# Kernel optimization log

Hardware: AMD Instinct MI355X
Metric: run time of the kernel (lower is better)

Reference implementation:

```python
import jax, jax.numpy as jnp
import numpy as np

S = 256
H = 4       # n_heads
DH = 32     # head_dim
D = H * DH  # model dim
EPS = 1e-5


def setup_inputs() -> dict:
    key = jax.random.key(0)
    ks = jax.random.split(key, 12)
    x = jax.random.normal(ks[0], (1, S, S, D), dtype=jnp.float32)
    # attention mask: mostly 0, occasionally large negative (masked)
    keep = jax.random.uniform(ks[1], (1, 1, S, S)) < 0.9
    attn_mask = jnp.where(keep, 0.0, -1e9).astype(jnp.float32)
    sc = 1.0 / np.sqrt(D)
    ln_w = jnp.ones((D,), jnp.float32)
    ln_b = jnp.zeros((D,), jnp.float32)
    Wb = jax.random.normal(ks[2], (H, D), jnp.float32) * sc   # bias projection (linear.weight)
    Wq = jax.random.normal(ks[3], (D, D), jnp.float32) * sc
    Wk = jax.random.normal(ks[4], (D, D), jnp.float32) * sc
    Wv = jax.random.normal(ks[5], (D, D), jnp.float32) * sc
    Wg = jax.random.normal(ks[6], (D, D), jnp.float32) * sc
    Wo = jax.random.normal(ks[7], (D, D), jnp.float32) * sc
    return {"x": x, "attn_mask": attn_mask, "ln_w": ln_w, "ln_b": ln_b,
            "Wb": Wb, "Wq": Wq, "Wk": Wk, "Wv": Wv, "Wg": Wg, "Wo": Wo}


def reference(x, attn_mask, ln_w, ln_b, Wb, Wq, Wk, Wv, Wg, Wo):
    # x: [1,S,S,D] pair representation; ending=False so no transpose of S axes.
    x0 = x[0]  # [S,S,D]
    mu = jnp.mean(x0, axis=-1, keepdims=True)
    var = jnp.mean(jnp.square(x0 - mu), axis=-1, keepdims=True)
    xn = (x0 - mu) * jax.lax.rsqrt(var + EPS) * ln_w + ln_b  # [S,S,D]

    # triangle bias: [S,S,H] -> [1,H,S,S] (broadcast over batch-of-rows)
    bias = jnp.einsum('bqd,hd->hbq', xn, Wb)[None]  # [1,H,S,S]

    def heads(W):
        return jnp.einsum('bqd,ed->bqe', xn, W).reshape(S, S, H, DH).transpose(0, 2, 1, 3)

    q, k, v = heads(Wq), heads(Wk), heads(Wv)  # each [S,H,S,DH]

    scale = 1.0 / np.sqrt(DH)
    scores = jnp.einsum('bhqd,bhkd->bhqk', q, k) * scale + bias + attn_mask  # [S,H,S,S]
    attn = jax.nn.softmax(scores, axis=-1)
    o = jnp.einsum('bhqk,bhkd->bhqd', attn, v)  # [S,H,S,DH]
    o = o.transpose(0, 2, 1, 3).reshape(S, S, D)

    g = jnp.einsum('bqd,ed->bqe', xn, Wg)
    out = jnp.einsum('bqe,fe->bqf', o * jax.nn.sigmoid(g), Wo)  # [S,S,D]
    return out[None]  # [1,S,S,D]
```

## Files before the change

kernel.cpp:

```cpp
#include <hip/hip_runtime.h>
#include <hip/hip_bf16.h>

#define S_DIM 256
#define D_DIM 128
#define H_DIM 4
#define NPOS  (S_DIM * S_DIM)
#define SW    384

typedef __attribute__((ext_vector_type(8))) short  short8;
typedef __attribute__((ext_vector_type(4))) float  f32x4;

__device__ __forceinline__ float b2f(unsigned short u) {
    union { float f; unsigned int u32; } c; c.u32 = ((unsigned int)u) << 16; return c.f;
}
__device__ __forceinline__ unsigned short f2b(float f) {
    __hip_bfloat16 h = __float2bfloat16(f);
    return *reinterpret_cast<unsigned short*>(&h);
}

__global__ __launch_bounds__(256) void ln_biasmask_kernel(
    const float* __restrict__ x, const float* __restrict__ mask,
    const float* __restrict__ lnw, const float* __restrict__ lnb,
    const float* __restrict__ Wb, float* __restrict__ bm)
{
    const int wave = threadIdx.x >> 6, lane = threadIdx.x & 63;
    const int p = blockIdx.x * 4 + wave;

    float2 v = ((const float2*)x)[p * 64 + lane];
    float s = v.x + v.y, ss = v.x * v.x + v.y * v.y;
    #pragma unroll
    for (int m = 1; m < 64; m <<= 1) { s += __shfl_xor(s, m); ss += __shfl_xor(ss, m); }
    float mean = s * (1.f / 128.f);
    float var  = ss * (1.f / 128.f) - mean * mean;
    float rstd = rsqrtf(var + 1e-5f);

    float xn0 = (v.x - mean) * rstd * lnw[lane * 2]     + lnb[lane * 2];
    float xn1 = (v.y - mean) * rstd * lnw[lane * 2 + 1] + lnb[lane * 2 + 1];

    float mval = mask[p];
    #pragma unroll
    for (int h = 0; h < H_DIM; h++) {
        float d = xn0 * Wb[h * 128 + lane * 2] + xn1 * Wb[h * 128 + lane * 2 + 1];
        #pragma unroll
        for (int m = 1; m < 64; m <<= 1) d += __shfl_xor(d, m);
        if (lane == 0) bm[(long)h * NPOS + p] = d + mval;
    }
}

__global__ __launch_bounds__(256) void proj_ln_kernel(
    const float* __restrict__ x,
    const float* __restrict__ lnw, const float* __restrict__ lnb,
    const float* __restrict__ Wq, const float* __restrict__ Wk,
    const float* __restrict__ Wv, const float* __restrict__ Wg,
    int p0, unsigned short* __restrict__ strip, unsigned short* __restrict__ vt)
{
    __shared__ __align__(16) unsigned short A_lds[64 * 136];
    __shared__ __align__(16) unsigned short W_lds[128 * 136];
    const int tid = threadIdx.x;
    const int m0 = blockIdx.x * 64;
    const int gy = blockIdx.y;
    const float* W = (gy == 0) ? Wq : (gy == 1) ? Wk : (gy == 2) ? Wv : Wg;

    const int lr = tid >> 4, c8 = (tid & 15) * 8;
    #pragma unroll
    for (int i = 0; i < 4; i++) {
        int row = lr + i * 16;
        const float* src = x + (size_t)(p0 + m0 + row) * 128 + c8;
        float4 f0 = *(const float4*)(src);
        float4 f1 = *(const float4*)(src + 4);
        float s  = f0.x + f0.y + f0.z + f0.w + f1.x + f1.y + f1.z + f1.w;
        float ss = f0.x*f0.x + f0.y*f0.y + f0.z*f0.z + f0.w*f0.w
                 + f1.x*f1.x + f1.y*f1.y + f1.z*f1.z + f1.w*f1.w;
        #pragma unroll
        for (int m = 1; m < 16; m <<= 1) { s += __shfl_xor(s, m); ss += __shfl_xor(ss, m); }
        float mean = s * (1.f / 128.f);
        float var  = ss * (1.f / 128.f) - mean * mean;
        float rstd = rsqrtf(var + 1e-5f);
        float xv[8] = {f0.x, f0.y, f0.z, f0.w, f1.x, f1.y, f1.z, f1.w};
        unsigned short pk[8];
        #pragma unroll
        for (int j = 0; j < 8; j++)
            pk[j] = f2b((xv[j] - mean) * rstd * lnw[c8 + j] + lnb[c8 + j]);
        *(uint4*)(&A_lds[row * 136 + c8]) = *(const uint4*)pk;
    }
    #pragma unroll
    for (int i = 0; i < 8; i++) {
        int wr = lr + i * 16;
        const float* src = W + (size_t)wr * 128 + c8;
        float4 f0 = *(const float4*)(src);
        float4 f1 = *(const float4*)(src + 4);
        unsigned short pk[8] = {f2b(f0.x), f2b(f0.y), f2b(f0.z), f2b(f0.w),
                                f2b(f1.x), f2b(f1.y), f2b(f1.z), f2b(f1.w)};
        *(uint4*)(&W_lds[wr * 136 + c8]) = *(const uint4*)pk;
    }
    __syncthreads();

    const int w = tid >> 6, lane = tid & 63;
    const int l16 = lane & 15, quad = lane >> 4;
    f32x4 acc[8];
    #pragma unroll
    for (int nt = 0; nt < 8; nt++) acc[nt] = (f32x4){0.f, 0.f, 0.f, 0.f};

    if (gy == 2) {
        #pragma unroll
        for (int k0 = 0; k0 < 128; k0 += 32) {
            short8 a = *(const short8*)(&A_lds[(w * 16 + l16) * 136 + k0 + quad * 8]);
            #pragma unroll
            for (int nt = 0; nt < 8; nt++) {
                short8 b = *(const short8*)(&W_lds[(nt * 16 + l16) * 136 + k0 + quad * 8]);
                acc[nt] = __builtin_amdgcn_mfma_f32_16x16x32_bf16(a, b, acc[nt], 0, 0, 0);
            }
        }
        const int blv = m0 >> 8;
        const int kl  = (m0 & 255) + w * 16 + quad * 4;
        #pragma unroll
        for (int nt = 0; nt < 8; nt++) {
            uint2 pk;
            pk.x = (unsigned)f2b(acc[nt][0]) | ((unsigned)f2b(acc[nt][1]) << 16);
            pk.y = (unsigned)f2b(acc[nt][2]) | ((unsigned)f2b(acc[nt][3]) << 16);
            *(uint2*)(&vt[((size_t)(blv * 128 + nt * 16 + l16)) * 256 + kl]) = pk;
        }
    } else {
        #pragma unroll
        for (int k0 = 0; k0 < 128; k0 += 32) {
            short8 a = *(const short8*)(&A_lds[(w * 16 + l16) * 136 + k0 + quad * 8]);
            #pragma unroll
            for (int nt = 0; nt < 8; nt++) {
                short8 b = *(const short8*)(&W_lds[(nt * 16 + l16) * 136 + k0 + quad * 8]);
                acc[nt] = __builtin_amdgcn_mfma_f32_16x16x32_bf16(b, a, acc[nt], 0, 0, 0);
            }
        }
        const int off = (gy == 0) ? 0 : (gy == 1) ? 128 : 256;
        const size_t rowbase = (size_t)(m0 + w * 16 + l16) * SW + off;
        #pragma unroll
        for (int nt = 0; nt < 8; nt++) {
            uint2 pk;
            pk.x = (unsigned)f2b(acc[nt][0]) | ((unsigned)f2b(acc[nt][1]) << 16);
            pk.y = (unsigned)f2b(acc[nt][2]) | ((unsigned)f2b(acc[nt][3]) << 16);
            *(uint2*)(&strip[rowbase + nt * 16 + quad * 4]) = pk;
        }
    }
}

__global__ __launch_bounds__(256) void attn_kernel(
    const unsigned short* __restrict__ strip, const unsigned short* __restrict__ vt,
    const float* __restrict__ bm, int b0, unsigned short* __restrict__ gated)
{
    __shared__ __align__(16) unsigned short P_lds[4 * 16 * 264];
    const int bl = blockIdx.x, h = blockIdx.y;
    const int b  = b0 + bl;
    const int tid = threadIdx.x;
    const int w = tid >> 6, lane = tid & 63;
    const int l16 = lane & 15, quad = lane >> 4;
    const float* bmh = bm + (long)h * NPOS;
    const unsigned short* vth = vt + ((size_t)bl * 128 + h * 32) * 256;
    unsigned short* P_w = P_lds + w * 16 * 264;
    const float scale = 0.17677669529663687f;

    #pragma unroll 1
    for (int i = 0; i < 4; i++) {
        const int q0 = (w * 4 + i) * 16;
        short8 bq = *(const short8*)(strip + (size_t)(bl * 256 + q0 + l16) * SW + h * 32 + quad * 8);
        const float* brow = bmh + (size_t)(q0 + l16) * 256 + quad * 4;

        float sc[16][4];
        #pragma unroll
        for (int nt = 0; nt < 16; nt++) {
            short8 ka = *(const short8*)(strip + (size_t)(bl * 256 + nt * 16 + l16) * SW + 128 + h * 32 + quad * 8);
            f32x4 c = (f32x4){0.f, 0.f, 0.f, 0.f};
            c = __builtin_amdgcn_mfma_f32_16x16x32_bf16(ka, bq, c, 0, 0, 0);
            float4 bb = *(const float4*)(brow + nt * 16);
            sc[nt][0] = c[0] * scale + bb.x;
            sc[nt][1] = c[1] * scale + bb.y;
            sc[nt][2] = c[2] * scale + bb.z;
            sc[nt][3] = c[3] * scale + bb.w;
        }

        float m0 = sc[0][0], m1 = sc[0][1], m2 = sc[0][2], m3 = sc[0][3];
        #pragma unroll
        for (int nt = 1; nt < 16; nt++) {
            m0 = fmaxf(m0, sc[nt][0]); m1 = fmaxf(m1, sc[nt][1]);
            m2 = fmaxf(m2, sc[nt][2]); m3 = fmaxf(m3, sc[nt][3]);
        }
        float m = fmaxf(fmaxf(m0, m1), fmaxf(m2, m3));
        m = fmaxf(m, __shfl_xor(m, 16));
        m = fmaxf(m, __shfl_xor(m, 32));

        float s0 = 0.f, s1 = 0.f, s2 = 0.f, s3 = 0.f;
        #pragma unroll
        for (int nt = 0; nt < 16; nt++) {
            float p0_ = __expf(sc[nt][0] - m); sc[nt][0] = p0_; s0 += p0_;
            float p1_ = __expf(sc[nt][1] - m); sc[nt][1] = p1_; s1 += p1_;
            float p2_ = __expf(sc[nt][2] - m); sc[nt][2] = p2_; s2 += p2_;
            float p3_ = __expf(sc[nt][3] - m); sc[nt][3] = p3_; s3 += p3_;
        }
        float ssum = (s0 + s1) + (s2 + s3);
        ssum += __shfl_xor(ssum, 16);
        ssum += __shfl_xor(ssum, 32);
        float inv = 1.f / ssum;

        #pragma unroll
        for (int nt = 0; nt < 16; nt++) {
            uint2 pk;
            pk.x = (unsigned)f2b(sc[nt][0]) | ((unsigned)f2b(sc[nt][1]) << 16);
            pk.y = (unsigned)f2b(sc[nt][2]) | ((unsigned)f2b(sc[nt][3]) << 16);
            *(uint2*)(&P_w[l16 * 264 + nt * 16 + quad * 4]) = pk;
        }

        f32x4 oacc[2];
        oacc[0] = (f32x4){0.f, 0.f, 0.f, 0.f};
        oacc[1] = (f32x4){0.f, 0.f, 0.f, 0.f};
        #pragma unroll
        for (int kt = 0; kt < 8; kt++) {
            short8 pa = *(const short8*)(&P_w[l16 * 264 + kt * 32 + quad * 8]);
            #pragma unroll
            for (int nh = 0; nh < 2; nh++) {
                short8 vb = *(const short8*)(vth + (size_t)(nh * 16 + l16) * 256 + kt * 32 + quad * 8);
                oacc[nh] = __builtin_amdgcn_mfma_f32_16x16x32_bf16(pa, vb, oacc[nh], 0, 0, 0);
            }
        }
        #pragma unroll
        for (int rr = 0; rr < 4; rr++) {
            float invr = __shfl(inv, quad * 4 + rr);
            int row = q0 + quad * 4 + rr;
            #pragma unroll
            for (int nh = 0; nh < 2; nh++) {
                int cl = nh * 16 + l16;
                float g = b2f(strip[(size_t)(bl * 256 + row) * SW + 256 + h * 32 + cl]);
                float ov = oacc[nh][rr] * invr;
                ov = ov / (1.f + __expf(-g));
                gated[((size_t)b * 256 + row) * 128 + h * 32 + cl] = f2b(ov);
            }
        }
    }
}

__global__ __launch_bounds__(256) void outproj_mfma_kernel(
    const unsigned short* __restrict__ gated, const float* __restrict__ Wo,
    float* __restrict__ out)
{
    __shared__ __align__(16) unsigned short A_lds[64 * 136];
    __shared__ __align__(16) unsigned short W_lds[128 * 136];
    const int tid = threadIdx.x;
    const int m0 = blockIdx.x * 64;

    const int lr = tid >> 4, c8 = (tid & 15) * 8;
    #pragma unroll
    for (int i = 0; i < 4; i++) {
        int row = lr + i * 16;
        *(uint4*)(&A_lds[row * 136 + c8]) =
            *(const uint4*)(gated + (size_t)(m0 + row) * 128 + c8);
    }
    #pragma unroll
    for (int i = 0; i < 8; i++) {
        const float* src = Wo + (size_t)(lr + i * 16) * 128 + c8;
        float4 f0 = *(const float4*)(src);
        float4 f1 = *(const float4*)(src + 4);
        unsigned short pk[8] = {f2b(f0.x), f2b(f0.y), f2b(f0.z), f2b(f0.w),
                                f2b(f1.x), f2b(f1.y), f2b(f1.z), f2b(f1.w)};
        *(uint4*)(&W_lds[(lr + i * 16) * 136 + c8]) = *(const uint4*)pk;
    }
    __syncthreads();

    const int w = tid >> 6, lane = tid & 63;
    const int l16 = lane & 15, quad = lane >> 4;
    f32x4 acc[8];
    #pragma unroll
    for (int nt = 0; nt < 8; nt++) acc[nt] = (f32x4){0.f, 0.f, 0.f, 0.f};

    #pragma unroll
    for (int k0 = 0; k0 < 128; k0 += 32) {
        short8 a = *(const short8*)(&A_lds[(w * 16 + l16) * 136 + k0 + quad * 8]);
        #pragma unroll
        for (int nt = 0; nt < 8; nt++) {
            short8 b = *(const short8*)(&W_lds[(nt * 16 + l16) * 136 + k0 + quad * 8]);
            acc[nt] = __builtin_amdgcn_mfma_f32_16x16x32_bf16(b, a, acc[nt], 0, 0, 0);
        }
    }

    float* orow = out + (size_t)(m0 + w * 16 + l16) * 128;
    #pragma unroll
    for (int nt = 0; nt < 8; nt++)
        *(f32x4*)(&orow[nt * 16 + quad * 4]) = acc[nt];
}

extern "C" void kernel_launch(void* const* d_in, const int* in_sizes, int n_in,
                              void* d_out, int out_size, void* d_ws, size_t ws_size,
                              hipStream_t stream)
{
    (void)in_sizes; (void)n_in; (void)out_size;
    const float* x    = (const float*)d_in[0];
    const float* mask = (const float*)d_in[1];
    const float* lnw  = (const float*)d_in[2];
    const float* lnb  = (const float*)d_in[3];
    const float* Wb   = (const float*)d_in[4];
    const float* Wq   = (const float*)d_in[5];
    const float* Wk   = (const float*)d_in[6];
    const float* Wv   = (const float*)d_in[7];
    const float* Wg   = (const float*)d_in[8];
    const float* Wo   = (const float*)d_in[9];
    float* out = (float*)d_out;

    const size_t bmB   = (size_t)H_DIM * NPOS * sizeof(float);
    const size_t gB    = (size_t)NPOS * 128 * sizeof(unsigned short);
    const size_t perRow = (size_t)256 * SW * 2 + (size_t)128 * 256 * 2;
    int HB = 256;
    while (HB > 16 && bmB + gB + (size_t)HB * perRow > ws_size) HB >>= 1;

    char* ws = (char*)d_ws;
    float*          bm    = (float*)ws;
    unsigned short* gated = (unsigned short*)(ws + bmB);
    unsigned short* vt    = (unsigned short*)(ws + bmB + gB);
    unsigned short* strip = vt + (size_t)HB * 128 * 256;

    ln_biasmask_kernel<<<NPOS / 4, 256, 0, stream>>>(x, mask, lnw, lnb, Wb, bm);
    for (int b0 = 0; b0 < S_DIM; b0 += HB) {
        proj_ln_kernel<<<dim3(HB * 4, 4), 256, 0, stream>>>(
            x, lnw, lnb, Wq, Wk, Wv, Wg, b0 * 256, strip, vt);
        attn_kernel<<<dim3(HB, H_DIM), 256, 0, stream>>>(strip, vt, bm, b0, gated);
    }
    outproj_mfma_kernel<<<NPOS / 64, 256, 0, stream>>>(gated, Wo, out);
}
```

Baseline: 241.7 us.

## Pre-convert weights once, fuse LN-bias into projection, stage K/V in LDS

Adds a small kernel that converts all five weight matrices to bf16 once, so the projection and output kernels read bf16 weights straight from global memory instead of reconverting them into LDS in every block. The projection kernel now loops over the four weight matrices inside one block, which removes the separate LayerNorm recompute per projection, and when the full workspace fits it also computes the triangle bias plus mask, replacing the standalone ln_biasmask kernel. The attention kernel stages K and V for its head in swizzled LDS and keeps the softmax probabilities in registers as packed bf16, dropping the P round trip through LDS. It also sets an occupancy hint on the attention kernel. The trade-offs are more serial work per projection block and weight B-operands fetched from L2 rather than LDS.

New measurement: 302.8 us. 25.3% more time.

```diff
diff --git a/kernel.cpp b/kernel.cpp
--- a/kernel.cpp
+++ b/kernel.cpp
@@ -18,6 +18,22 @@
     return *reinterpret_cast<unsigned short*>(&h);
 }
 
+__global__ __launch_bounds__(256) void wconv_kernel(
+    const float* __restrict__ Wq, const float* __restrict__ Wk,
+    const float* __restrict__ Wv, const float* __restrict__ Wg,
+    const float* __restrict__ Wo, unsigned short* __restrict__ wbf)
+{
+    const int gy = blockIdx.y;
+    const float* W = (gy == 0) ? Wq : (gy == 1) ? Wk : (gy == 2) ? Wv
+                   : (gy == 3) ? Wg : Wo;
+    const int idx = (blockIdx.x * 256 + threadIdx.x) * 8;
+    float4 f0 = *(const float4*)(W + idx);
+    float4 f1 = *(const float4*)(W + idx + 4);
+    unsigned short pk[8] = {f2b(f0.x), f2b(f0.y), f2b(f0.z), f2b(f0.w),
+                            f2b(f1.x), f2b(f1.y), f2b(f1.z), f2b(f1.w)};
+    *(uint4*)(wbf + (size_t)gy * 16384 + idx) = *(const uint4*)pk;
+}
+
 __global__ __launch_bounds__(256) void ln_biasmask_kernel(
     const float* __restrict__ x, const float* __restrict__ mask,
     const float* __restrict__ lnw, const float* __restrict__ lnb,
@@ -47,25 +63,33 @@
     }
 }
 
+template<int FUSE_BIAS>
 __global__ __launch_bounds__(256) void proj_ln_kernel(
-    const float* __restrict__ x,
+    const float* __restrict__ x, const float* __restrict__ mask,
     const float* __restrict__ lnw, const float* __restrict__ lnb,
-    const float* __restrict__ Wq, const float* __restrict__ Wk,
-    const float* __restrict__ Wv, const float* __restrict__ Wg,
-    int p0, unsigned short* __restrict__ strip, unsigned short* __restrict__ vt)
+    const float* __restrict__ Wb, const unsigned short* __restrict__ wbf,
+    int p0, unsigned short* __restrict__ strip, unsigned short* __restrict__ vt,
+    float* __restrict__ bm)
 {
     __shared__ __align__(16) unsigned short A_lds[64 * 136];
-    __shared__ __align__(16) unsigned short W_lds[128 * 136];
     const int tid = threadIdx.x;
     const int m0 = blockIdx.x * 64;
-    const int gy = blockIdx.y;
-    const float* W = (gy == 0) ? Wq : (gy == 1) ? Wk : (gy == 2) ? Wv : Wg;
-
     const int lr = tid >> 4, c8 = (tid & 15) * 8;
+
+    float4 wb0[4], wb1[4];
+    if (FUSE_BIAS) {
+        #pragma unroll
+        for (int hh = 0; hh < 4; hh++) {
+            wb0[hh] = *(const float4*)(Wb + hh * 128 + c8);
+            wb1[hh] = *(const float4*)(Wb + hh * 128 + c8 + 4);
+        }
+    }
+
     #pragma unroll
     for (int i = 0; i < 4; i++) {
         int row = lr + i * 16;
-        const float* src = x + (size_t)(p0 + m0 + row) * 128 + c8;
+        int p   = p0 + m0 + row;
+        const float* src = x + (size_t)p * 128 + c8;
         float4 f0 = *(const float4*)(src);
         float4 f1 = *(const float4*)(src + 4);
         float s  = f0.x + f0.y + f0.z + f0.w + f1.x + f1.y + f1.z + f1.w;
@@ -77,98 +101,137 @@
         float var  = ss * (1.f / 128.f) - mean * mean;
         float rstd = rsqrtf(var + 1e-5f);
         float xv[8] = {f0.x, f0.y, f0.z, f0.w, f1.x, f1.y, f1.z, f1.w};
+        float xl[8];
         unsigned short pk[8];
         #pragma unroll
-        for (int j = 0; j < 8; j++)
-            pk[j] = f2b((xv[j] - mean) * rstd * lnw[c8 + j] + lnb[c8 + j]);
+        for (int j = 0; j < 8; j++) {
+            xl[j] = (xv[j] - mean) * rstd * lnw[c8 + j] + lnb[c8 + j];
+            pk[j] = f2b(xl[j]);
+        }
         *(uint4*)(&A_lds[row * 136 + c8]) = *(const uint4*)pk;
-    }
-    #pragma unroll
-    for (int i = 0; i < 8; i++) {
-        int wr = lr + i * 16;
-        const float* src = W + (size_t)wr * 128 + c8;
-        float4 f0 = *(const float4*)(src);
-        float4 f1 = *(const float4*)(src + 4);
-        unsigned short pk[8] = {f2b(f0.x), f2b(f0.y), f2b(f0.z), f2b(f0.w),
-                                f2b(f1.x), f2b(f1.y), f2b(f1.z), f2b(f1.w)};
-        *(uint4*)(&W_lds[wr * 136 + c8]) = *(const uint4*)pk;
+
+        if (FUSE_BIAS) {
+            float mv = 0.f;
+            if ((tid & 15) == 0) mv = mask[p];
+            #pragma unroll
+            for (int hh = 0; hh < 4; hh++) {
+                float bh = xl[0]*wb0[hh].x + xl[1]*wb0[hh].y
+                         + xl[2]*wb0[hh].z + xl[3]*wb0[hh].w
+                         + xl[4]*wb1[hh].x + xl[5]*wb1[hh].y
+                         + xl[6]*wb1[hh].z + xl[7]*wb1[hh].w;
+                #pragma unroll
+                for (int mk = 1; mk < 16; mk <<= 1) bh += __shfl_xor(bh, mk);
+                if ((tid & 15) == 0) bm[(long)hh * NPOS + p] = bh + mv;
+            }
+        }
     }
     __syncthreads();
 
     const int w = tid >> 6, lane = tid & 63;
     const int l16 = lane & 15, quad = lane >> 4;
-    f32x4 acc[8];
-    #pragma unroll
-    for (int nt = 0; nt < 8; nt++) acc[nt] = (f32x4){0.f, 0.f, 0.f, 0.f};
-
-    if (gy == 2) {
-        #pragma unroll
-        for (int k0 = 0; k0 < 128; k0 += 32) {
-            short8 a = *(const short8*)(&A_lds[(w * 16 + l16) * 136 + k0 + quad * 8]);
+
+    short8 a4[4];
+    #pragma unroll
+    for (int k0i = 0; k0i < 4; k0i++)
+        a4[k0i] = *(const short8*)(&A_lds[(w * 16 + l16) * 136 + k0i * 32 + quad * 8]);
+
+    #pragma unroll 1
+    for (int gy = 0; gy < 4; gy++) {
+        const unsigned short* Wg_ = wbf + (size_t)gy * 16384;
+        f32x4 acc[8];
+        #pragma unroll
+        for (int nt = 0; nt < 8; nt++) acc[nt] = (f32x4){0.f, 0.f, 0.f, 0.f};
+
+        if (gy == 2) {
+            #pragma unroll
+            for (int k0i = 0; k0i < 4; k0i++)
+                #pragma unroll
+                for (int nt = 0; nt < 8; nt++) {
+                    short8 b = *(const short8*)(Wg_ + (size_t)(nt * 16 + l16) * 128 + k0i * 32 + quad * 8);
+                    acc[nt] = __builtin_amdgcn_mfma_f32_16x16x32_bf16(a4[k0i], b, acc[nt], 0, 0, 0);
+                }
+            const int blv = m0 >> 8;
+            const int kl  = (m0 & 255) + w * 16 + quad * 4;
             #pragma unroll
             for (int nt = 0; nt < 8; nt++) {
-                short8 b = *(const short8*)(&W_lds[(nt * 16 + l16) * 136 + k0 + quad * 8]);
-                acc[nt] = __builtin_amdgcn_mfma_f32_16x16x32_bf16(a, b, acc[nt], 0, 0, 0);
-            }
-        }
-        const int blv = m0 >> 8;
-        const int kl  = (m0 & 255) + w * 16 + quad * 4;
-        #pragma unroll
-        for (int nt = 0; nt < 8; nt++) {
-            uint2 pk;
-            pk.x = (unsigned)f2b(acc[nt][0]) | ((unsigned)f2b(acc[nt][1]) << 16);
-            pk.y = (unsigned)f2b(acc[nt][2]) | ((unsigned)f2b(acc[nt][3]) << 16);
-            *(uint2*)(&vt[((size_t)(blv * 128 + nt * 16 + l16)) * 256 + kl]) = pk;
-        }
-    } else {
-        #pragma unroll
-        for (int k0 = 0; k0 < 128; k0 += 32) {
-            short8 a = *(const short8*)(&A_lds[(w * 16 + l16) * 136 + k0 + quad * 8]);
+                uint2 pk;
+                pk.x = (unsigned)f2b(acc[nt][0]) | ((unsigned)f2b(acc[nt][1]) << 16);
+                pk.y = (unsigned)f2b(acc[nt][2]) | ((unsigned)f2b(acc[nt][3]) << 16);
+                *(uint2*)(&vt[((size_t)(blv * 128 + nt * 16 + l16)) * 256 + kl]) = pk;
+            }
+        } else {
+            #pragma unroll
+            for (int k0i = 0; k0i < 4; k0i++)
+                #pragma unroll
+                for (int nt = 0; nt < 8; nt++) {
+                    short8 b = *(const short8*)(Wg_ + (size_t)(nt * 16 + l16) * 128 + k0i * 32 + quad * 8);
+                    acc[nt] = __builtin_amdgcn_mfma_f32_16x16x32_bf16(b, a4[k0i], acc[nt], 0, 0, 0);
+                }
+            const int off = (gy == 0) ? 0 : (gy == 1) ? 128 : 256;
+            const size_t rowbase = (size_t)(m0 + w * 16 + l16) * SW + off;
             #pragma unroll
             for (int nt = 0; nt < 8; nt++) {
-                short8 b = *(const short8*)(&W_lds[(nt * 16 + l16) * 136 + k0 + quad * 8]);
-                acc[nt] = __builtin_amdgcn_mfma_f32_16x16x32_bf16(b, a, acc[nt], 0, 0, 0);
-            }
-        }
-        const int off = (gy == 0) ? 0 : (gy == 1) ? 128 : 256;
-        const size_t rowbase = (size_t)(m0 + w * 16 + l16) * SW + off;
-        #pragma unroll
-        for (int nt = 0; nt < 8; nt++) {
-            uint2 pk;
-            pk.x = (unsigned)f2b(acc[nt][0]) | ((unsigned)f2b(acc[nt][1]) << 16);
-            pk.y = (unsigned)f2b(acc[nt][2]) | ((unsigned)f2b(acc[nt][3]) << 16);
-            *(uint2*)(&strip[rowbase + nt * 16 + quad * 4]) = pk;
-        }
-    }
-}
-
-__global__ __launch_bounds__(256) void attn_kernel(
+                uint2 pk;
+                pk.x = (unsigned)f2b(acc[nt][0]) | ((unsigned)f2b(acc[nt][1]) << 16);
+                pk.y = (unsigned)f2b(acc[nt][2]) | ((unsigned)f2b(acc[nt][3]) << 16);
+                *(uint2*)(&strip[rowbase + nt * 16 + quad * 4]) = pk;
+            }
+        }
+    }
+}
+
+__global__ __launch_bounds__(256, 4) void attn_kernel(
     const unsigned short* __restrict__ strip, const unsigned short* __restrict__ vt,
     const float* __restrict__ bm, int b0, unsigned short* __restrict__ gated)
 {
-    __shared__ __align__(16) unsigned short P_lds[4 * 16 * 264];
+    __shared__ __align__(16) unsigned short K_lds[16 * 4 * 16 * 8];
+    __shared__ __align__(16) unsigned short V_lds[8 * 4 * 2 * 16 * 8];
     const int bl = blockIdx.x, h = blockIdx.y;
     const int b  = b0 + bl;
     const int tid = threadIdx.x;
+
+    #pragma unroll
+    for (int i = 0; i < 4; i++) {
+        int r = i * 64 + (tid >> 2), c = tid & 3;
+        uint4 v = *(const uint4*)(strip + (size_t)(bl * 256 + r) * SW + 128 + h * 32 + c * 8);
+        *(uint4*)(&K_lds[(((r >> 4) * 4 + c) * 16 + (r & 15)) * 8]) = v;
+    }
+    #pragma unroll
+    for (int i = 0; i < 4; i++) {
+        int d = tid >> 3, m = (tid & 7) + i * 8;
+        uint4 v = *(const uint4*)(vt + ((size_t)(bl * 128 + h * 32 + d)) * 256 + m * 8);
+        int base = (((m >> 2) * 4 + (m & 1) * 2) * 2 + (d >> 4)) * 128
+                 + (d & 15) * 8 + ((m >> 1) & 1) * 4;
+        uint2 lo; lo.x = v.x; lo.y = v.y;
+        uint2 hi; hi.x = v.z; hi.y = v.w;
+        *(uint2*)(&V_lds[base])       = lo;
+        *(uint2*)(&V_lds[base + 256]) = hi;
+    }
+    __syncthreads();
+
     const int w = tid >> 6, lane = tid & 63;
     const int l16 = lane & 15, quad = lane >> 4;
     const float* bmh = bm + (long)h * NPOS;
-    const unsigned short* vth = vt + ((size_t)bl * 128 + h * 32) * 256;
-    unsigned short* P_w = P_lds + w * 16 * 264;
     const float scale = 0.17677669529663687f;
 
+    short8 bq4[4];
+    #pragma unroll
+    for (int i = 0; i < 4; i++) {
+        int q0 = (w * 4 + i) * 16;
+        bq4[i] = *(const short8*)(strip + (size_t)(bl * 256 + q0 + l16) * SW + h * 32 + quad * 8);
+    }
+
     #pragma unroll 1
     for (int i = 0; i < 4; i++) {
         const int q0 = (w * 4 + i) * 16;
-        short8 bq = *(const short8*)(strip + (size_t)(bl * 256 + q0 + l16) * SW + h * 32 + quad * 8);
         const float* brow = bmh + (size_t)(q0 + l16) * 256 + quad * 4;
 
         float sc[16][4];
         #pragma unroll
         for (int nt = 0; nt < 16; nt++) {
-            short8 ka = *(const short8*)(strip + (size_t)(bl * 256 + nt * 16 + l16) * SW + 128 + h * 32 + quad * 8);
+            short8 ka = *(const short8*)(&K_lds[((nt * 4 + quad) * 16 + l16) * 8]);
             f32x4 c = (f32x4){0.f, 0.f, 0.f, 0.f};
-            c = __builtin_amdgcn_mfma_f32_16x16x32_bf16(ka, bq, c, 0, 0, 0);
+            c = __builtin_amdgcn_mfma_f32_16x16x32_bf16(ka, bq4[i], c, 0, 0, 0);
             float4 bb = *(const float4*)(brow + nt * 16);
             sc[nt][0] = c[0] * scale + bb.x;
             sc[nt][1] = c[1] * scale + bb.y;
@@ -176,46 +239,44 @@
             sc[nt][3] = c[3] * scale + bb.w;
         }
 
-        float m0 = sc[0][0], m1 = sc[0][1], m2 = sc[0][2], m3 = sc[0][3];
+        float m0_ = sc[0][0], m1_ = sc[0][1], m2_ = sc[0][2], m3_ = sc[0][3];
         #pragma unroll
         for (int nt = 1; nt < 16; nt++) {
-            m0 = fmaxf(m0, sc[nt][0]); m1 = fmaxf(m1, sc[nt][1]);
-            m2 = fmaxf(m2, sc[nt][2]); m3 = fmaxf(m3, sc[nt][3]);
-        }
-        float m = fmaxf(fmaxf(m0, m1), fmaxf(m2, m3));
+            m0_ = fmaxf(m0_, sc[nt][0]); m1_ = fmaxf(m1_, sc[nt][1]);
+            m2_ = fmaxf(m2_, sc[nt][2]); m3_ = fmaxf(m3_, sc[nt][3]);
+        }
+        float m = fmaxf(fmaxf(m0_, m1_), fmaxf(m2_, m3_));
         m = fmaxf(m, __shfl_xor(m, 16));
         m = fmaxf(m, __shfl_xor(m, 32));
 
         float s0 = 0.f, s1 = 0.f, s2 = 0.f, s3 = 0.f;
+        unsigned int pk[32];
         #pragma unroll
         for (int nt = 0; nt < 16; nt++) {
-            float p0_ = __expf(sc[nt][0] - m); sc[nt][0] = p0_; s0 += p0_;
-            float p1_ = __expf(sc[nt][1] - m); sc[nt][1] = p1_; s1 += p1_;
-            float p2_ = __expf(sc[nt][2] - m); sc[nt][2] = p2_; s2 += p2_;
-            float p3_ = __expf(sc[nt][3] - m); sc[nt][3] = p3_; s3 += p3_;
+            float p0_ = __expf(sc[nt][0] - m); s0 += p0_;
+            float p1_ = __expf(sc[nt][1] - m); s1 += p1_;
+            float p2_ = __expf(sc[nt][2] - m); s2 += p2_;
+            float p3_ = __expf(sc[nt][3] - m); s3 += p3_;
+            pk[nt * 2]     = (unsigned)f2b(p0_) | ((unsigned)f2b(p1_) << 16);
+            pk[nt * 2 + 1] = (unsigned)f2b(p2_) | ((unsigned)f2b(p3_) << 16);
         }
         float ssum = (s0 + s1) + (s2 + s3);
         ssum += __shfl_xor(ssum, 16);
         ssum += __shfl_xor(ssum, 32);
         float inv = 1.f / ssum;
 
-        #pragma unroll
-        for (int nt = 0; nt < 16; nt++) {
-            uint2 pk;
-            pk.x = (unsigned)f2b(sc[nt][0]) | ((unsigned)f2b(sc[nt][1]) << 16);
-            pk.y = (unsigned)f2b(sc[nt][2]) | ((unsigned)f2b(sc[nt][3]) << 16);
-            *(uint2*)(&P_w[l16 * 264 + nt * 16 + quad * 4]) = pk;
-        }
-
         f32x4 oacc[2];
         oacc[0] = (f32x4){0.f, 0.f, 0.f, 0.f};
         oacc[1] = (f32x4){0.f, 0.f, 0.f, 0.f};
         #pragma unroll
         for (int kt = 0; kt < 8; kt++) {
-            short8 pa = *(const short8*)(&P_w[l16 * 264 + kt * 32 + quad * 8]);
+            union { unsigned int u[4]; short8 s; } pu;
+            pu.u[0] = pk[kt * 4];     pu.u[1] = pk[kt * 4 + 1];
+            pu.u[2] = pk[kt * 4 + 2]; pu.u[3] = pk[kt * 4 + 3];
+            short8 pa = pu.s;
             #pragma unroll
             for (int nh = 0; nh < 2; nh++) {
-                short8 vb = *(const short8*)(vth + (size_t)(nh * 16 + l16) * 256 + kt * 32 + quad * 8);
+                short8 vb = *(const short8*)(&V_lds[(((kt * 4 + quad) * 2 + nh) * 16 + l16) * 8]);
                 oacc[nh] = __builtin_amdgcn_mfma_f32_16x16x32_bf16(pa, vb, oacc[nh], 0, 0, 0);
             }
         }
@@ -236,47 +297,31 @@
 }
 
 __global__ __launch_bounds__(256) void outproj_mfma_kernel(
-    const unsigned short* __restrict__ gated, const float* __restrict__ Wo,
+    const unsigned short* __restrict__ gated, const unsigned short* __restrict__ wbf,
     float* __restrict__ out)
 {
-    __shared__ __align__(16) unsigned short A_lds[64 * 136];
-    __shared__ __align__(16) unsigned short W_lds[128 * 136];
-    const int tid = threadIdx.x;
-    const int m0 = blockIdx.x * 64;
-
-    const int lr = tid >> 4, c8 = (tid & 15) * 8;
-    #pragma unroll
-    for (int i = 0; i < 4; i++) {
-        int row = lr + i * 16;
-        *(uint4*)(&A_lds[row * 136 + c8]) =
-            *(const uint4*)(gated + (size_t)(m0 + row) * 128 + c8);
-    }
-    #pragma unroll
-    for (int i = 0; i < 8; i++) {
-        const float* src = Wo + (size_t)(lr + i * 16) * 128 + c8;
-        float4 f0 = *(const float4*)(src);
-        float4 f1 = *(const float4*)(src + 4);
-        unsigned short pk[8] = {f2b(f0.x), f2b(f0.y), f2b(f0.z), f2b(f0.w),
-                                f2b(f1.x), f2b(f1.y), f2b(f1.z), f2b(f1.w)};
-        *(uint4*)(&W_lds[(lr + i * 16) * 136 + c8]) = *(const uint4*)pk;
-    }
-    __syncthreads();
-
+    const int tid = threadIdx.x, m0 = blockIdx.x * 64;
     const int w = tid >> 6, lane = tid & 63;
     const int l16 = lane & 15, quad = lane >> 4;
+    const unsigned short* Wo = wbf + (size_t)4 * 16384;
+
+    const unsigned short* arow = gated + (size_t)(m0 + w * 16 + l16) * 128;
+    short8 a4[4];
+    #pragma unroll
+    for (int k0i = 0; k0i < 4; k0i++)
+        a4[k0i] = *(const short8*)(arow + k0i * 32 + quad * 8);
+
     f32x4 acc[8];
     #pragma unroll
     for (int nt = 0; nt < 8; nt++) acc[nt] = (f32x4){0.f, 0.f, 0.f, 0.f};
 
     #pragma unroll
-    for (int k0 = 0; k0 < 128; k0 += 32) {
-        short8 a = *(const short8*)(&A_lds[(w * 16 + l16) * 136 + k0 + quad * 8]);
+    for (int k0i = 0; k0i < 4; k0i++)
         #pragma unroll
         for (int nt = 0; nt < 8; nt++) {
-            short8 b = *(const short8*)(&W_lds[(nt * 16 + l16) * 136 + k0 + quad * 8]);
-            acc[nt] = __builtin_amdgcn_mfma_f32_16x16x32_bf16(b, a, acc[nt], 0, 0, 0);
-        }
-    }
+            short8 b = *(const short8*)(Wo + (size_t)(nt * 16 + l16) * 128 + k0i * 32 + quad * 8);
+            acc[nt] = __builtin_amdgcn_mfma_f32_16x16x32_bf16(b, a4[k0i], acc[nt], 0, 0, 0);
+        }
 
     float* orow = out + (size_t)(m0 + w * 16 + l16) * 128;
     #pragma unroll
@@ -301,23 +346,33 @@
     const float* Wo   = (const float*)d_in[9];
     float* out = (float*)d_out;
 
-    const size_t bmB   = (size_t)H_DIM * NPOS * sizeof(float);
-    const size_t gB    = (size_t)NPOS * 128 * sizeof(unsigned short);
+    const size_t bmB = (size_t)H_DIM * NPOS * sizeof(float);
+    const size_t gB  = (size_t)NPOS * 128 * sizeof(unsigned short);
+    const size_t wB  = (size_t)5 * 16384 * sizeof(unsigned short);
     const size_t perRow = (size_t)256 * SW * 2 + (size_t)128 * 256 * 2;
     int HB = 256;
-    while (HB > 16 && bmB + gB + (size_t)HB * perRow > ws_size) HB >>= 1;
+    while (HB > 16 && bmB + gB + wB + (size_t)HB * perRow > ws_size) HB >>= 1;
 
     char* ws = (char*)d_ws;
     float*          bm    = (float*)ws;
     unsigned short* gated = (unsigned short*)(ws + bmB);
-    unsigned short* vt    = (unsigned short*)(ws + bmB + gB);
+    unsigned short* wbf   = (unsigned short*)(ws + bmB + gB);
+    unsigned short* vt    = (unsigned short*)(ws + bmB + gB + wB);
     unsigned short* strip = vt + (size_t)HB * 128 * 256;
 
-    ln_biasmask_kernel<<<NPOS / 4, 256, 0, stream>>>(x, mask, lnw, lnb, Wb, bm);
-    for (int b0 = 0; b0 < S_DIM; b0 += HB) {
-        proj_ln_kernel<<<dim3(HB * 4, 4), 256, 0, stream>>>(
-            x, lnw, lnb, Wq, Wk, Wv, Wg, b0 * 256, strip, vt);
-        attn_kernel<<<dim3(HB, H_DIM), 256, 0, stream>>>(strip, vt, bm, b0, gated);
-    }
-    outproj_mfma_kernel<<<NPOS / 64, 256, 0, stream>>>(gated, Wo, out);
-}
+    wconv_kernel<<<dim3(8, 5), 256, 0, stream>>>(Wq, Wk, Wv, Wg, Wo, wbf);
+
+    if (HB == 256) {
+        proj_ln_kernel<1><<<dim3(256 * 4), 256, 0, stream>>>(
+            x, mask, lnw, lnb, Wb, wbf, 0, strip, vt, bm);
+        attn_kernel<<<dim3(256, H_DIM), 256, 0, stream>>>(strip, vt, bm, 0, gated);
+    } else {
+        ln_biasmask_kernel<<<NPOS / 4, 256, 0, stream>>>(x, mask, lnw, lnb, Wb, bm);
+        for (int b0 = 0; b0 < S_DIM; b0 += HB) {
+            proj_ln_kernel<0><<<dim3(HB * 4), 256, 0, stream>>>(
+                x, mask, lnw, lnb, Wb, wbf, b0 * 256, strip, vt, bm);
+            attn_kernel<<<dim3(HB, H_DIM), 256, 0, stream>>>(strip, vt, bm, b0, gated);
+        }
+    }
+    outproj_mfma_kernel<<<NPOS / 64, 256, 0, stream>>>(gated, wbf, out);
+}
```
